# Optimization experiments

Hardware: AMD Instinct MI355X
Metric: run time of the kernel (lower is better)

## Reference

```python
import jax, jax.numpy as jnp
import numpy as np


def _normalize_adj(edge_index, num_nodes):
    # add self loops
    loop = jnp.arange(num_nodes, dtype=edge_index.dtype)
    row = jnp.concatenate([edge_index[0], loop])
    col = jnp.concatenate([edge_index[1], loop])
    deg = jax.ops.segment_sum(jnp.ones(row.shape[0], jnp.float32), row,
                              num_segments=num_nodes)
    dis = jnp.where(deg > 0, jax.lax.rsqrt(deg), 0.0)  # deg^{-1/2}, inf->0
    ew = dis[row] * dis[col]
    return row, col, ew


def _gcn_conv(x, W, b, row, col, ew, num_nodes):
    h = x @ W.T + b                       # dense linear [N, out]
    msg = h[col] * ew[:, None]            # gather + scale [E', out]
    return jax.ops.segment_sum(msg, row, num_segments=num_nodes)  # scatter_add


def setup_inputs() -> dict:
    N, E, IN, HID, OUT = 100000, 1600000, 128, 128, 64
    key = jax.random.key(0)
    k1, k2, k3, k4 = jax.random.split(key, 4)
    x = jax.random.normal(k1, (N, IN), jnp.float32)
    edge_index = jax.random.randint(k2, (2, E), 0, N, jnp.int64)
    # xavier_uniform for weights, zero bias (as in reset_parameters)
    lim1 = float(np.sqrt(6.0 / (IN + HID)))
    lim2 = float(np.sqrt(6.0 / (HID + OUT)))
    W1 = jax.random.uniform(k3, (HID, IN), jnp.float32, -lim1, lim1)
    b1 = jnp.zeros((HID,), jnp.float32)
    W2 = jax.random.uniform(k4, (OUT, HID), jnp.float32, -lim2, lim2)
    b2 = jnp.zeros((OUT,), jnp.float32)
    return {"x": x, "edge_index": edge_index, "num_nodes": N,
            "W1": W1, "b1": b1, "W2": W2, "b2": b2}


def reference(x, edge_index, num_nodes, W1, b1, W2, b2):
    row, col, ew = _normalize_adj(edge_index, num_nodes)
    h = _gcn_conv(x, W1, b1, row, col, ew, num_nodes)
    h = jax.nn.relu(h)  # dropout is identity in eval mode
    out = _gcn_conv(h, W2, b2, row, col, ew, num_nodes)
    return out
```

## Files before the change

kernel.cpp:

```cpp
#include <hip/hip_runtime.h>
#include <hip/hip_bf16.h>
#include <stdint.h>


#define TPB 256
#define NBLK_C 256
#define TPB_C 1024
#define MAX_NB 2048

typedef __attribute__((ext_vector_type(8))) __bf16 bf16x8;
typedef __attribute__((ext_vector_type(4))) float f32x4;
typedef __attribute__((ext_vector_type(2))) float f32x2;
typedef __attribute__((ext_vector_type(4))) unsigned int u32x4;

__device__ __forceinline__ float bf16lo(unsigned u) { return __uint_as_float(u << 16); }
__device__ __forceinline__ float bf16hi(unsigned u) { return __uint_as_float(u & 0xffff0000u); }
__device__ __forceinline__ unsigned short f2bf(float f) {
    unsigned u = __float_as_uint(f);
    return (unsigned short)((u + 0x7fff + ((u >> 16) & 1)) >> 16);
}
__device__ __forceinline__ f32x2 pk_add(f32x2 a, f32x2 b) {
    f32x2 d;
    asm("v_pk_add_f32 %0, %1, %2" : "=v"(d) : "v"(a), "v"(b));
    return d;
}

__global__ __launch_bounds__(TPB_C) void hist_extract_kernel(const void* __restrict__ ei, int E,
                                                             int CH,
                                                             int* __restrict__ row32,
                                                             int* __restrict__ col32,
                                                             int* __restrict__ hist,
                                                             int NB, int N) {
    __shared__ int h[MAX_NB];
    __shared__ int s_is64;
    int tid = threadIdx.x;
    if (tid < 64) {
        int x = ((const int*)ei)[2 * tid + 1];
        unsigned long long b = __ballot(x != 0);
        if (tid == 0) s_is64 = (b == 0ull);
    }
    for (int bin = tid; bin < NB; bin += TPB_C) h[bin] = 0;
    __syncthreads();

    int b = blockIdx.x;
    int s = b * CH;
    int end = min(E, s + CH);
    int is64 = s_is64;
    unsigned uN = (unsigned)N;
    if (is64) {
        const long long* p = (const long long*)ei;
        for (int e = s + tid; e < end; e += TPB_C) {
            int r = (int)p[e];
            int c = (int)p[E + e];
            row32[e] = r;
            col32[e] = c;
            if ((unsigned)r < uN && (unsigned)c < uN) atomicAdd(&h[r >> 7], 1);
        }
    } else {
        const int* p = (const int*)ei;
        for (int e = s + tid; e < end; e += TPB_C) {
            int r = p[e];
            int c = p[E + e];
            row32[e] = r;
            col32[e] = c;
            if ((unsigned)r < uN && (unsigned)c < uN) atomicAdd(&h[r >> 7], 1);
        }
    }
    __syncthreads();
    for (int bin = tid; bin < NB; bin += TPB_C) hist[bin * NBLK_C + b] = h[bin];
}

__global__ __launch_bounds__(NBLK_C) void colscan_kernel(int* __restrict__ hist,
                                                         int* __restrict__ binTotal) {
    __shared__ int sm[NBLK_C];
    int bin = blockIdx.x;
    int tid = threadIdx.x;
    int v = hist[bin * NBLK_C + tid];
    sm[tid] = v;
    __syncthreads();
    for (int o = 1; o < NBLK_C; o <<= 1) {
        int x = (tid >= o) ? sm[tid - o] : 0;
        __syncthreads();
        sm[tid] += x;
        __syncthreads();
    }
    hist[bin * NBLK_C + tid] = sm[tid] - v;
    if (tid == NBLK_C - 1) binTotal[bin] = sm[NBLK_C - 1];
}

__global__ __launch_bounds__(TPB_C) void scatter_kernel(const int* __restrict__ row32,
                                                        const int* __restrict__ col32, int E,
                                                        int CH,
                                                        const int* __restrict__ hist,
                                                        const int* __restrict__ binTotal,
                                                        int* __restrict__ bucketed,
                                                        int NB, int N) {
    __shared__ int cur[MAX_NB];
    __shared__ int sm2[TPB_C];
    int tid = threadIdx.x;
    int b = blockIdx.x;

    int v = (tid < NB) ? binTotal[tid] : 0;
    sm2[tid] = v;
    __syncthreads();
    for (int o = 1; o < TPB_C; o <<= 1) {
        int x = (tid >= o) ? sm2[tid - o] : 0;
        __syncthreads();
        sm2[tid] += x;
        __syncthreads();
    }
    if (tid < NB) cur[tid] = (sm2[tid] - v) + hist[tid * NBLK_C + b];
    __syncthreads();

    int s = b * CH;
    int end = min(E, s + CH);
    unsigned uN = (unsigned)N;
    for (int e = s + tid; e < end; e += TPB_C) {
        int r = row32[e];
        int c = col32[e];
        if ((unsigned)r < uN && (unsigned)c < uN) {
            int pos = atomicAdd(&cur[r >> 7], 1);
            bucketed[pos] = (c << 7) | (r & 127);
        }
    }
}

__global__ __launch_bounds__(TPB) void finecsr_kernel(const int* __restrict__ bucketed,
                                                      const int* __restrict__ binTotal,
                                                      int4* __restrict__ meta,
                                                      float* __restrict__ dis,
                                                      int* __restrict__ csr, int N) {
    __shared__ int c128[128];
    __shared__ int cur128[128];
    __shared__ int sm[TPB];
    __shared__ int red[TPB];
    int bin = blockIdx.x;
    int tid = threadIdx.x;

    int part = 0;
    for (int i = tid; i < bin; i += TPB) part += binTotal[i];
    red[tid] = part;
    __syncthreads();
    for (int o = TPB / 2; o > 0; o >>= 1) {
        if (tid < o) red[tid] += red[tid + o];
        __syncthreads();
    }
    int s = red[0];
    int m = binTotal[bin];

    if (tid < 128) c128[tid] = 0;
    __syncthreads();
    for (int i = tid; i < m; i += TPB) atomicAdd(&c128[bucketed[s + i] & 127], 1);
    __syncthreads();

    int v = (tid < 128) ? c128[tid] : 0;
    sm[tid] = v;
    __syncthreads();
    for (int o = 1; o < 128; o <<= 1) {
        int x = (tid >= o) ? sm[tid - o] : 0;
        __syncthreads();
        sm[tid] += x;
        __syncthreads();
    }
    if (tid < 128) {
        int excl = sm[tid] - v;
        int r = bin * 128 + tid;
        if (r < N) {
            float dv = rsqrtf((float)v + 1.0f);
            meta[r] = make_int4(s + excl, v, __float_as_int(dv), 0);
            dis[r] = dv;
        }
        cur128[tid] = s + excl;
    }
    __syncthreads();
    for (int i = tid; i < m; i += TPB) {
        int p = bucketed[s + i];
        int pos = atomicAdd(&cur128[p & 127], 1);
        csr[pos] = p >> 7;
    }
}

template <int BN, bool INB16>
__global__ __launch_bounds__(256, 2) void gemm_mfma_kernel(const void* __restrict__ Xp,
                                                           const float* __restrict__ W,
                                                           const float* __restrict__ bias,
                                                           const float* __restrict__ dis,
                                                           unsigned short* __restrict__ Hb,
                                                           int N) {
    constexpr int XST = 136;
    __shared__ unsigned short Xs[128 * XST];
    __shared__ unsigned short Ws[BN * XST];

    const int tid = threadIdx.x;
    const int r0 = blockIdx.x * 128;

    if (blockIdx.x == 0 && tid < (BN >> 1))
        ((unsigned*)Hb)[(size_t)N * (BN >> 1) + tid] = 0u;

    if (INB16) {
        const ushort4* Xv = (const ushort4*)Xp;
        for (int idx = tid; idx < 128 * 32; idx += 256) {
            int row = idx >> 5, q = idx & 31;
            int rg = r0 + row;
            if (rg >= N) rg = N - 1;
            *(ushort4*)&Xs[row * XST + q * 4] = Xv[(size_t)rg * 32 + q];
        }
    } else {
        const float4* Xv = (const float4*)Xp;
        for (int idx = tid; idx < 128 * 32; idx += 256) {
            int row = idx >> 5, q = idx & 31;
            int rg = r0 + row;
            if (rg >= N) rg = N - 1;
            float4 v = Xv[(size_t)rg * 32 + q];
            ushort4 s = make_ushort4(f2bf(v.x), f2bf(v.y), f2bf(v.z), f2bf(v.w));
            *(ushort4*)&Xs[row * XST + q * 4] = s;
        }
    }
    {
        const float4* Wv = (const float4*)W;
        for (int idx = tid; idx < BN * 32; idx += 256) {
            int n = idx >> 5, q = idx & 31;
            float4 v = Wv[n * 32 + q];
            ushort4 s = make_ushort4(f2bf(v.x), f2bf(v.y), f2bf(v.z), f2bf(v.w));
            *(ushort4*)&Ws[n * XST + q * 4] = s;
        }
    }
    __syncthreads();

    constexpr int RT = (BN == 128) ? 4 : 2;
    constexpr int CT = 4;
    const int wave = tid >> 6, lane = tid & 63;
    const int l15 = lane & 15, q8 = lane >> 4;
    const int row0 = (BN == 128) ? (wave & 1) * 64 : wave * 32;
    const int col0 = (BN == 128) ? (wave >> 1) * 64 : 0;

    f32x4 zero = {0.f, 0.f, 0.f, 0.f};
    f32x4 acc[RT][CT];
#pragma unroll
    for (int rt = 0; rt < RT; ++rt)
#pragma unroll
        for (int ct = 0; ct < CT; ++ct) acc[rt][ct] = zero;

#pragma unroll
    for (int ks = 0; ks < 4; ++ks) {
        int ko = ks * 32 + q8 * 8;
        bf16x8 a[RT], b[CT];
#pragma unroll
        for (int rt = 0; rt < RT; ++rt)
            a[rt] = *(const bf16x8*)&Xs[(row0 + rt * 16 + l15) * XST + ko];
#pragma unroll
        for (int ct = 0; ct < CT; ++ct)
            b[ct] = *(const bf16x8*)&Ws[(col0 + ct * 16 + l15) * XST + ko];
#pragma unroll
        for (int rt = 0; rt < RT; ++rt)
#pragma unroll
            for (int ct = 0; ct < CT; ++ct)
                acc[rt][ct] = __builtin_amdgcn_mfma_f32_16x16x32_bf16(
                    a[rt], b[ct], acc[rt][ct], 0, 0, 0);
    }

    float bv[CT];
#pragma unroll
    for (int ct = 0; ct < CT; ++ct) bv[ct] = bias[col0 + ct * 16 + l15];
#pragma unroll
    for (int rt = 0; rt < RT; ++rt)
#pragma unroll
        for (int r = 0; r < 4; ++r) {
            int row = r0 + row0 + rt * 16 + q8 * 4 + r;
            if (row < N) {
                float dn = dis[row];
#pragma unroll
                for (int ct = 0; ct < CT; ++ct)
                    Hb[(size_t)row * BN + col0 + ct * 16 + l15] =
                        f2bf((acc[rt][ct][r] + bv[ct]) * dn);
            }
        }
}

template <int F, bool RELU, bool OB16, bool NTLD, bool NTST>
__global__ __launch_bounds__(TPB) void agg_kernel(const unsigned short* __restrict__ Hb,
                                                  const int* __restrict__ csr,
                                                  const int4* __restrict__ meta,
                                                  void* __restrict__ outp, int N) {
    constexpr int RS = F / 2;
    constexpr int LPR = RS / 4;
    constexpr int G = 64 / LPR;
    constexpr int KQ = 16 / G;
    constexpr int NW = 4;

    int w = (blockIdx.x * TPB + threadIdx.x) >> 6;
    if (w >= N) return;
    const int lane = threadIdx.x & 63;
    const int g = lane / LPR;
    const int fl = lane % LPR;

    int4 m = meta[w];
    const int s = m.x, d = m.y;
    const float di = __int_as_float(m.z);

    const unsigned* Hu = (const unsigned*)Hb;

    f32x2 acc2[NW];
#pragma unroll
    for (int t = 0; t < NW; ++t) acc2[t] = (f32x2){0.f, 0.f};

    auto accum_row = [&](const unsigned (&u)[NW]) {
#pragma unroll
        for (int t = 0; t < NW; ++t) {
            f32x2 lh;
            lh.x = bf16lo(u[t]);
            lh.y = bf16hi(u[t]);
            acc2[t] = pk_add(acc2[t], lh);
        }
    };
    auto load_row = [&](unsigned (&u)[NW], int r) {
        u32x4 v = *(const u32x4*)(Hu + (size_t)r * RS + fl * NW);
        u[0] = v.x; u[1] = v.y; u[2] = v.z; u[3] = v.w;
    };

    if (g == 0) {
        unsigned su[NW];
        load_row(su, w);
        accum_row(su);
    }

    for (int base = 0; base < d; base += 64) {
        int rem = d - base;
        if (rem > 64) rem = 64;
        int cl;
        if (lane < rem) {
            if constexpr (NTLD) cl = __builtin_nontemporal_load(csr + s + base + lane);
            else                cl = csr[s + base + lane];
        } else cl = 0;

        for (int e = 0; e < rem; e += 32) {
            int cc0[KQ];
#pragma unroll
            for (int k = 0; k < KQ; ++k) {
                int idx = e + k * G + g;
                int raw = __shfl(cl, idx & 63);
                cc0[k] = (idx < rem) ? raw : N;
            }
            unsigned u0[KQ][NW];
#pragma unroll
            for (int k = 0; k < KQ; ++k) load_row(u0[k], cc0[k]);

            const bool two = (e + 16) < rem;
            int cc1[KQ];
            unsigned u1[KQ][NW];
            if (two) {
#pragma unroll
                for (int k = 0; k < KQ; ++k) {
                    int idx = e + 16 + k * G + g;
                    int raw = __shfl(cl, idx & 63);
                    cc1[k] = (idx < rem) ? raw : N;
                }
#pragma unroll
                for (int k = 0; k < KQ; ++k) load_row(u1[k], cc1[k]);
            }
#pragma unroll
            for (int k = 0; k < KQ; ++k) accum_row(u0[k]);
            if (two) {
#pragma unroll
                for (int k = 0; k < KQ; ++k) accum_row(u1[k]);
            }
        }
    }

#pragma unroll
    for (int off = LPR; off < 64; off <<= 1)
#pragma unroll
        for (int t = 0; t < NW; ++t) {
            acc2[t].x += __shfl_xor(acc2[t].x, off);
            acc2[t].y += __shfl_xor(acc2[t].y, off);
        }

#pragma unroll
    for (int t = 0; t < NW; ++t) {
        acc2[t].x *= di;
        acc2[t].y *= di;
        if (RELU) {
            acc2[t].x = fmaxf(acc2[t].x, 0.0f);
            acc2[t].y = fmaxf(acc2[t].y, 0.0f);
        }
    }

    if (lane < LPR) {
        if constexpr (OB16) {
            u32x4 dw;
            dw.x = (unsigned)f2bf(acc2[0].x) | ((unsigned)f2bf(acc2[0].y) << 16);
            dw.y = (unsigned)f2bf(acc2[1].x) | ((unsigned)f2bf(acc2[1].y) << 16);
            dw.z = (unsigned)f2bf(acc2[2].x) | ((unsigned)f2bf(acc2[2].y) << 16);
            dw.w = (unsigned)f2bf(acc2[3].x) | ((unsigned)f2bf(acc2[3].y) << 16);
            unsigned* op = (unsigned*)outp;
            u32x4* dst = (u32x4*)(op + (size_t)w * RS + fl * NW);
            if constexpr (NTST) __builtin_nontemporal_store(dw, dst);
            else                *dst = dw;
        } else {
            f32x4 v0 = {acc2[0].x, acc2[0].y, acc2[1].x, acc2[1].y};
            f32x4 v1 = {acc2[2].x, acc2[2].y, acc2[3].x, acc2[3].y};
            f32x4* op = (f32x4*)outp;
            f32x4* d0 = op + (size_t)w * (F / 4) + fl * 2;
            if constexpr (NTST) {
                __builtin_nontemporal_store(v0, d0);
                __builtin_nontemporal_store(v1, d0 + 1);
            } else {
                d0[0] = v0;
                d0[1] = v1;
            }
        }
    }
}

extern "C" void kernel_launch(void* const* d_in, const int* in_sizes, int n_in,
                              void* d_out, int out_size, void* d_ws, size_t ws_size,
                              hipStream_t stream) {
    const float* x  = (const float*)d_in[0];
    const void*  ei = d_in[1];
    const float* W1 = (const float*)d_in[3];
    const float* b1 = (const float*)d_in[4];
    const float* W2 = (const float*)d_in[5];
    const float* b2 = (const float*)d_in[6];
    float* out = (float*)d_out;

    const int IN = 128, HID = 128;
    const int N = in_sizes[0] / IN;
    const int E = in_sizes[1] / 2;
    const int NB = (N + 127) >> 7;
    const int CH = (E + NBLK_C - 1) / NBLK_C;

    char* ws = (char*)d_ws;
    size_t off = 0;
    auto alloc = [&](size_t bytes) -> void* {
        void* p = (void*)(ws + off);
        off += (bytes + 255) & ~(size_t)255;
        return p;
    };
    int4*  meta     = (int4*)alloc((size_t)N * 16);
    float* dis      = (float*)alloc((size_t)N * 4);
    int*   row32    = (int*)alloc((size_t)E * 4);
    int*   col32    = (int*)alloc((size_t)E * 4);
    int*   bucketed = (int*)alloc((size_t)E * 4);
    int*   csr      = (int*)alloc((size_t)E * 4);
    int*   hist     = (int*)alloc((size_t)NB * NBLK_C * 4);
    int*   binTotal = (int*)alloc((size_t)NB * 4);
    unsigned short* H1b = (unsigned short*)alloc((size_t)(N + 1) * HID * 2);
    unsigned short* R1b = (unsigned short*)alloc((size_t)(N + 1) * HID * 2);
    unsigned short* H2b = H1b;

    hist_extract_kernel<<<NBLK_C, TPB_C, 0, stream>>>(ei, E, CH, row32, col32,
                                                      hist, NB, N);
    colscan_kernel<<<NB, NBLK_C, 0, stream>>>(hist, binTotal);
    scatter_kernel<<<NBLK_C, TPB_C, 0, stream>>>(row32, col32, E, CH, hist, binTotal,
                                                 bucketed, NB, N);
    finecsr_kernel<<<NB, TPB, 0, stream>>>(bucketed, binTotal, meta, dis, csr, N);

    int ngrid = (N + 127) / 128;
    int agrid = (N + 3) / 4;

    gemm_mfma_kernel<128, false><<<ngrid, 256, 0, stream>>>(x, W1, b1, dis, H1b, N);
    agg_kernel<128, true, true, false, false><<<agrid, TPB, 0, stream>>>(H1b, csr, meta,
                                                                         R1b, N);

    gemm_mfma_kernel<64, true><<<ngrid, 256, 0, stream>>>(R1b, W2, b2, dis, H2b, N);
    agg_kernel<64, false, false, true, true><<<agrid, TPB, 0, stream>>>(H2b, csr, meta,
                                                                        out, N);
}
```

Measured before the change: 281.1 us.

## Fuse CSR build stages into one cooperative kernel with grid syncs

Merges the histogram/extract, column scan, scatter and fine-CSR kernels into a single cooperative kernel separated by grid-wide syncs. This removes three kernel launch boundaries and their gaps. In exchange, the column scan and fine CSR phases now run on only 256 blocks looping over the 782 bins, with 1024-thread blocks where many threads idle during the 128-wide scans. That lowers parallelism in those phases.

```diff
diff --git a/kernel.cpp b/kernel.cpp
--- a/kernel.cpp
+++ b/kernel.cpp
@@ -1,6 +1,9 @@
 #include <hip/hip_runtime.h>
 #include <hip/hip_bf16.h>
+#include <hip/hip_cooperative_groups.h>
 #include <stdint.h>
+
+namespace cg = cooperative_groups;
 
 
 #define TPB 256
@@ -25,158 +28,145 @@
     return d;
 }
 
-__global__ __launch_bounds__(TPB_C) void hist_extract_kernel(const void* __restrict__ ei, int E,
-                                                             int CH,
-                                                             int* __restrict__ row32,
-                                                             int* __restrict__ col32,
-                                                             int* __restrict__ hist,
-                                                             int NB, int N) {
+__global__ __launch_bounds__(TPB_C) void csrbuild_kernel(const void* __restrict__ ei, int E,
+                                                         int CH,
+                                                         int* __restrict__ row32,
+                                                         int* __restrict__ col32,
+                                                         int* __restrict__ hist,
+                                                         int* __restrict__ binTotal,
+                                                         int4* __restrict__ meta,
+                                                         float* __restrict__ dis,
+                                                         int* __restrict__ bucketed,
+                                                         int* __restrict__ csr,
+                                                         int NB, int N) {
+    cg::grid_group grid = cg::this_grid();
     __shared__ int h[MAX_NB];
+    __shared__ int sm[TPB_C];
+    __shared__ int c128[128];
+    __shared__ int cur128[128];
+    __shared__ int scn[128];
     __shared__ int s_is64;
-    int tid = threadIdx.x;
+
+    const int tid = threadIdx.x;
+    const int b = blockIdx.x;
+    const unsigned uN = (unsigned)N;
+
     if (tid < 64) {
         int x = ((const int*)ei)[2 * tid + 1];
-        unsigned long long b = __ballot(x != 0);
-        if (tid == 0) s_is64 = (b == 0ull);
+        unsigned long long bl = __ballot(x != 0);
+        if (tid == 0) s_is64 = (bl == 0ull);
     }
     for (int bin = tid; bin < NB; bin += TPB_C) h[bin] = 0;
     __syncthreads();
-
-    int b = blockIdx.x;
-    int s = b * CH;
-    int end = min(E, s + CH);
-    int is64 = s_is64;
-    unsigned uN = (unsigned)N;
-    if (is64) {
-        const long long* p = (const long long*)ei;
-        for (int e = s + tid; e < end; e += TPB_C) {
-            int r = (int)p[e];
-            int c = (int)p[E + e];
-            row32[e] = r;
-            col32[e] = c;
-            if ((unsigned)r < uN && (unsigned)c < uN) atomicAdd(&h[r >> 7], 1);
-        }
-    } else {
-        const int* p = (const int*)ei;
-        for (int e = s + tid; e < end; e += TPB_C) {
-            int r = p[e];
-            int c = p[E + e];
-            row32[e] = r;
-            col32[e] = c;
-            if ((unsigned)r < uN && (unsigned)c < uN) atomicAdd(&h[r >> 7], 1);
+    {
+        int s = b * CH;
+        int end = min(E, s + CH);
+        if (s_is64) {
+            const long long* p = (const long long*)ei;
+            for (int e = s + tid; e < end; e += TPB_C) {
+                int r = (int)p[e];
+                int c = (int)p[E + e];
+                row32[e] = r;
+                col32[e] = c;
+                if ((unsigned)r < uN && (unsigned)c < uN) atomicAdd(&h[r >> 7], 1);
+            }
+        } else {
+            const int* p = (const int*)ei;
+            for (int e = s + tid; e < end; e += TPB_C) {
+                int r = p[e];
+                int c = p[E + e];
+                row32[e] = r;
+                col32[e] = c;
+                if ((unsigned)r < uN && (unsigned)c < uN) atomicAdd(&h[r >> 7], 1);
+            }
         }
     }
     __syncthreads();
     for (int bin = tid; bin < NB; bin += TPB_C) hist[bin * NBLK_C + b] = h[bin];
-}
-
-__global__ __launch_bounds__(NBLK_C) void colscan_kernel(int* __restrict__ hist,
-                                                         int* __restrict__ binTotal) {
-    __shared__ int sm[NBLK_C];
-    int bin = blockIdx.x;
-    int tid = threadIdx.x;
-    int v = hist[bin * NBLK_C + tid];
-    sm[tid] = v;
+    __threadfence();
+    grid.sync();
+
+    for (int bin = b; bin < NB; bin += NBLK_C) {
+        int v = (tid < NBLK_C) ? hist[bin * NBLK_C + tid] : 0;
+        if (tid < NBLK_C) sm[tid] = v;
+        __syncthreads();
+        for (int o = 1; o < NBLK_C; o <<= 1) {
+            int x = (tid >= o && tid < NBLK_C) ? sm[tid - o] : 0;
+            __syncthreads();
+            if (tid < NBLK_C) sm[tid] += x;
+            __syncthreads();
+        }
+        if (tid < NBLK_C) hist[bin * NBLK_C + tid] = sm[tid] - v;
+        if (tid == NBLK_C - 1) binTotal[bin] = sm[NBLK_C - 1];
+        __syncthreads();
+    }
+    __threadfence();
+    grid.sync();
+
+    {
+        int v = (tid < NB) ? binTotal[tid] : 0;
+        sm[tid] = v;
+        __syncthreads();
+        for (int o = 1; o < TPB_C; o <<= 1) {
+            int x = (tid >= o) ? sm[tid - o] : 0;
+            __syncthreads();
+            sm[tid] += x;
+            __syncthreads();
+        }
+        if (tid < NB) h[tid] = (sm[tid] - v) + hist[tid * NBLK_C + b];
+    }
     __syncthreads();
-    for (int o = 1; o < NBLK_C; o <<= 1) {
-        int x = (tid >= o) ? sm[tid - o] : 0;
-        __syncthreads();
-        sm[tid] += x;
-        __syncthreads();
-    }
-    hist[bin * NBLK_C + tid] = sm[tid] - v;
-    if (tid == NBLK_C - 1) binTotal[bin] = sm[NBLK_C - 1];
-}
-
-__global__ __launch_bounds__(TPB_C) void scatter_kernel(const int* __restrict__ row32,
-                                                        const int* __restrict__ col32, int E,
-                                                        int CH,
-                                                        const int* __restrict__ hist,
-                                                        const int* __restrict__ binTotal,
-                                                        int* __restrict__ bucketed,
-                                                        int NB, int N) {
-    __shared__ int cur[MAX_NB];
-    __shared__ int sm2[TPB_C];
-    int tid = threadIdx.x;
-    int b = blockIdx.x;
-
-    int v = (tid < NB) ? binTotal[tid] : 0;
-    sm2[tid] = v;
-    __syncthreads();
-    for (int o = 1; o < TPB_C; o <<= 1) {
-        int x = (tid >= o) ? sm2[tid - o] : 0;
-        __syncthreads();
-        sm2[tid] += x;
-        __syncthreads();
-    }
-    if (tid < NB) cur[tid] = (sm2[tid] - v) + hist[tid * NBLK_C + b];
-    __syncthreads();
-
-    int s = b * CH;
-    int end = min(E, s + CH);
-    unsigned uN = (unsigned)N;
-    for (int e = s + tid; e < end; e += TPB_C) {
-        int r = row32[e];
-        int c = col32[e];
-        if ((unsigned)r < uN && (unsigned)c < uN) {
-            int pos = atomicAdd(&cur[r >> 7], 1);
-            bucketed[pos] = (c << 7) | (r & 127);
-        }
-    }
-}
-
-__global__ __launch_bounds__(TPB) void finecsr_kernel(const int* __restrict__ bucketed,
-                                                      const int* __restrict__ binTotal,
-                                                      int4* __restrict__ meta,
-                                                      float* __restrict__ dis,
-                                                      int* __restrict__ csr, int N) {
-    __shared__ int c128[128];
-    __shared__ int cur128[128];
-    __shared__ int sm[TPB];
-    __shared__ int red[TPB];
-    int bin = blockIdx.x;
-    int tid = threadIdx.x;
-
-    int part = 0;
-    for (int i = tid; i < bin; i += TPB) part += binTotal[i];
-    red[tid] = part;
-    __syncthreads();
-    for (int o = TPB / 2; o > 0; o >>= 1) {
-        if (tid < o) red[tid] += red[tid + o];
-        __syncthreads();
-    }
-    int s = red[0];
-    int m = binTotal[bin];
-
-    if (tid < 128) c128[tid] = 0;
-    __syncthreads();
-    for (int i = tid; i < m; i += TPB) atomicAdd(&c128[bucketed[s + i] & 127], 1);
-    __syncthreads();
-
-    int v = (tid < 128) ? c128[tid] : 0;
-    sm[tid] = v;
-    __syncthreads();
-    for (int o = 1; o < 128; o <<= 1) {
-        int x = (tid >= o) ? sm[tid - o] : 0;
-        __syncthreads();
-        sm[tid] += x;
-        __syncthreads();
-    }
-    if (tid < 128) {
-        int excl = sm[tid] - v;
-        int r = bin * 128 + tid;
-        if (r < N) {
-            float dv = rsqrtf((float)v + 1.0f);
-            meta[r] = make_int4(s + excl, v, __float_as_int(dv), 0);
-            dis[r] = dv;
-        }
-        cur128[tid] = s + excl;
-    }
-    __syncthreads();
-    for (int i = tid; i < m; i += TPB) {
-        int p = bucketed[s + i];
-        int pos = atomicAdd(&cur128[p & 127], 1);
-        csr[pos] = p >> 7;
+
+    {
+        int s = b * CH;
+        int end = min(E, s + CH);
+        for (int e = s + tid; e < end; e += TPB_C) {
+            int r = row32[e];
+            int c = col32[e];
+            if ((unsigned)r < uN && (unsigned)c < uN) {
+                int pos = atomicAdd(&h[r >> 7], 1);
+                bucketed[pos] = (c << 7) | (r & 127);
+            }
+        }
+    }
+    __threadfence();
+    grid.sync();
+
+    for (int bin = b; bin < NB; bin += NBLK_C) {
+        int m = binTotal[bin];
+        int s = sm[bin] - m;
+
+        if (tid < 128) c128[tid] = 0;
+        __syncthreads();
+        for (int i = tid; i < m; i += TPB_C) atomicAdd(&c128[bucketed[s + i] & 127], 1);
+        __syncthreads();
+
+        int v = (tid < 128) ? c128[tid] : 0;
+        if (tid < 128) scn[tid] = v;
+        __syncthreads();
+        for (int o = 1; o < 128; o <<= 1) {
+            int x = (tid >= o && tid < 128) ? scn[tid - o] : 0;
+            __syncthreads();
+            if (tid < 128) scn[tid] += x;
+            __syncthreads();
+        }
+        if (tid < 128) {
+            int excl = scn[tid] - v;
+            int r = bin * 128 + tid;
+            if (r < N) {
+                float dv = rsqrtf((float)v + 1.0f);
+                meta[r] = make_int4(s + excl, v, __float_as_int(dv), 0);
+                dis[r] = dv;
+            }
+            cur128[tid] = s + excl;
+        }
+        __syncthreads();
+        for (int i = tid; i < m; i += TPB_C) {
+            int p = bucketed[s + i];
+            int pos = atomicAdd(&cur128[p & 127], 1);
+            csr[pos] = p >> 7;
+        }
+        __syncthreads();
     }
 }
 
@@ -415,8 +405,8 @@
 extern "C" void kernel_launch(void* const* d_in, const int* in_sizes, int n_in,
                               void* d_out, int out_size, void* d_ws, size_t ws_size,
                               hipStream_t stream) {
+    const void*  ei = d_in[1];
     const float* x  = (const float*)d_in[0];
-    const void*  ei = d_in[1];
     const float* W1 = (const float*)d_in[3];
     const float* b1 = (const float*)d_in[4];
     const float* W2 = (const float*)d_in[5];
@@ -448,12 +438,16 @@
     unsigned short* R1b = (unsigned short*)alloc((size_t)(N + 1) * HID * 2);
     unsigned short* H2b = H1b;
 
-    hist_extract_kernel<<<NBLK_C, TPB_C, 0, stream>>>(ei, E, CH, row32, col32,
-                                                      hist, NB, N);
-    colscan_kernel<<<NB, NBLK_C, 0, stream>>>(hist, binTotal);
-    scatter_kernel<<<NBLK_C, TPB_C, 0, stream>>>(row32, col32, E, CH, hist, binTotal,
-                                                 bucketed, NB, N);
-    finecsr_kernel<<<NB, TPB, 0, stream>>>(bucketed, binTotal, meta, dis, csr, N);
+    {
+        void* kargs[] = {(void*)&ei, (void*)&E, (void*)&CH,
+                         (void*)&row32, (void*)&col32,
+                         (void*)&hist, (void*)&binTotal,
+                         (void*)&meta, (void*)&dis,
+                         (void*)&bucketed, (void*)&csr,
+                         (void*)&NB, (void*)&N};
+        hipLaunchCooperativeKernel((void*)csrbuild_kernel, dim3(NBLK_C), dim3(TPB_C),
+                                   kargs, 0, stream);
+    }
 
     int ngrid = (N + 127) / 128;
     int agrid = (N + 3) / 4;
```

After: 685.7 us. 2.44x slower.
